# Kernel optimization log

Measured on AMD Instinct MI355X. Metric: run time of the kernel, lower is better.

The kernel has to match this reference:

```python
import jax, jax.numpy as jnp
import numpy as np

TOP_K = 2


def setup_inputs() -> dict:
    key = jax.random.key(0)
    k0, k1, k2, k3, k4, k5 = jax.random.split(key, 6)
    N, D_IN, D_OUT, H, G = 8192, 1024, 1024, 4096, 3
    E = 2 ** G
    x = jax.random.normal(k0, (N, D_IN), jnp.float32)
    # gate: Linear(in_dim, gate_dim, bias=False) followed by act (ReLU)
    Wg = jax.random.normal(k1, (D_IN, G), jnp.float32) * (1.0 / np.sqrt(D_IN))
    # experts: per-expert 2-layer MLP: Linear(in,hid) + ReLU + Linear(hid,out)
    W1 = jax.random.normal(k2, (E, D_IN, H), jnp.float32) * (1.0 / np.sqrt(D_IN))
    b1 = jax.random.normal(k3, (E, H), jnp.float32) * 0.01
    W2 = jax.random.normal(k4, (E, H, D_OUT), jnp.float32) * (1.0 / np.sqrt(H))
    b2 = jax.random.normal(k5, (E, D_OUT), jnp.float32) * 0.01
    return {"x": x, "Wg": Wg, "W1": W1, "b1": b1, "W2": W2, "b2": b2}


def _hypercube_mask(E, G, dtype):
    # binary(arange(2^G), G) * 2 - 1 : corners of the hypercube in {-1,+1}^G
    codes = jnp.arange(E)
    bits = (codes[:, None] >> jnp.arange(G)[None, :]) & 1  # [E, G]
    return (bits * 2 - 1).astype(dtype)


def reference(x, Wg, W1, b1, W2, b2):
    G = Wg.shape[1]
    E = W1.shape[0]
    N = x.shape[0]
    mask = _hypercube_mask(E, G, x.dtype)                 # [E, G]
    logits = jax.nn.relu(x @ Wg)                          # [N, G]
    scores = logits @ mask.T                              # [N, E] = sum_d logits*mask
    probs = jax.nn.softmax(scores, axis=1)                # softmax over experts
    topv, topi = jax.lax.top_k(probs, TOP_K)              # [N, k]
    topv = topv / topv.sum(axis=-1, keepdims=True)        # renormalize selected probs
    # dense combine weights: zero for non-selected experts (same math as gather/scatter dispatch)
    combine = jnp.zeros((N, E), x.dtype).at[jnp.arange(N)[:, None], topi].set(topv)
    out = jnp.zeros((N, W2.shape[2]), x.dtype)
    for e in range(E):  # small fixed expert count
        h = jax.nn.relu(x @ W1[e] + b1[e])                # [N, H]
        out = out + combine[:, e:e + 1] * (h @ W2[e] + b2[e])
    return out
```

## Files before the change

kernel.cpp:

```cpp
#include <hip/hip_runtime.h>

#define NTOK 8192
#define DIN  1024
#define DOUT 1024
#define HDIM 4096
#define NEXP 8
#define NPAIR (NTOK * 2)

typedef __attribute__((ext_vector_type(8))) short bf16x8;
typedef __attribute__((ext_vector_type(4))) float f32x4;

__device__ __forceinline__ unsigned short f2bf(float f) {
  union { float f; unsigned u; } v; v.f = f;
  unsigned u = v.u;
  unsigned r = (u + 0x7fffu + ((u >> 16) & 1u)) >> 16;
  return (unsigned short)r;
}

__device__ __forceinline__ void gload16(const void* g, void* l) {
  __builtin_amdgcn_global_load_lds(
      (const __attribute__((address_space(1))) unsigned int*)g,
      (__attribute__((address_space(3))) unsigned int*)l, 16, 0, 0);
}

__global__ void gate_kernel(const float* __restrict__ x, const float* __restrict__ Wg,
                            int* __restrict__ cnt, int* __restrict__ ptok,
                            float* __restrict__ pw) {
  const int lane = threadIdx.x & 63;
  const int t = blockIdx.x * 4 + (threadIdx.x >> 6);
  const float* xr = x + (size_t)t * DIN + lane * 16;
  const float* wr = Wg + (size_t)lane * 16 * 3;
  double d0 = 0, d1 = 0, d2 = 0;
#pragma unroll
  for (int j = 0; j < 16; j++) {
    double xv = xr[j];
    d0 += xv * wr[j * 3 + 0];
    d1 += xv * wr[j * 3 + 1];
    d2 += xv * wr[j * 3 + 2];
  }
#pragma unroll
  for (int o = 32; o > 0; o >>= 1) {
    d0 += __shfl_down(d0, o);
    d1 += __shfl_down(d1, o);
    d2 += __shfl_down(d2, o);
  }
  if (lane == 0) {
    double l0 = d0 > 0 ? d0 : 0, l1 = d1 > 0 ? d1 : 0, l2 = d2 > 0 ? d2 : 0;
    double s[NEXP];
#pragma unroll
    for (int e = 0; e < NEXP; e++)
      s[e] = ((e & 1) ? l0 : -l0) + ((e & 2) ? l1 : -l1) + ((e & 4) ? l2 : -l2);
    int e0 = 0;
    for (int e = 1; e < NEXP; e++) if (s[e] > s[e0]) e0 = e;
    int e1 = -1;
    for (int e = 0; e < NEXP; e++) { if (e == e0) continue; if (e1 < 0 || s[e] > s[e1]) e1 = e; }
    double w0 = 1.0 / (1.0 + exp(s[e1] - s[e0]));
    double w1 = 1.0 - w0;
    int p0 = atomicAdd(cnt + e0, 1);
    ptok[e0 * NTOK + p0] = t; pw[e0 * NTOK + p0] = (float)w0;
    int p1 = atomicAdd(cnt + e1, 1);
    ptok[e1 * NTOK + p1] = t; pw[e1 * NTOK + p1] = (float)w1;
  }
}

__global__ void scan_kernel(const int* __restrict__ cnt, int* __restrict__ off) {
  if (threadIdx.x == 0) {
    int a = 0;
    for (int e = 0; e < NEXP; e++) { off[e] = a; a += cnt[e]; }
  }
}

__global__ void cvt_bf16_kernel(const float* __restrict__ src,
                                unsigned short* __restrict__ dst, int n) {
  int i = (blockIdx.x * 256 + threadIdx.x) * 8;
  if (i >= n) return;
  float4 a = *(const float4*)(src + i);
  float4 b = *(const float4*)(src + i + 4);
  __align__(16) unsigned short t[8] = {f2bf(a.x), f2bf(a.y), f2bf(a.z), f2bf(a.w),
                                       f2bf(b.x), f2bf(b.y), f2bf(b.z), f2bf(b.w)};
  *(uint4*)(dst + i) = *(const uint4*)t;
}

__global__ void transpose_cvt(const float* __restrict__ src,
                              unsigned short* __restrict__ dst, int K, int N) {
  __shared__ float tile[64][65];
  const size_t base = (size_t)blockIdx.z * K * N;
  const float* s = src + base;
  unsigned short* d = dst + base;
  int n0 = blockIdx.x * 64, k0 = blockIdx.y * 64;
  for (int idx = threadIdx.x; idx < 64 * 16; idx += 256) {
    int r = idx >> 4, c4 = (idx & 15) * 4;
    float4 v = *(const float4*)(s + (size_t)(k0 + r) * N + n0 + c4);
    tile[r][c4 + 0] = v.x; tile[r][c4 + 1] = v.y;
    tile[r][c4 + 2] = v.z; tile[r][c4 + 3] = v.w;
  }
  __syncthreads();
  for (int idx = threadIdx.x; idx < 64 * 8; idx += 256) {
    int nl = idx >> 3, c8 = (idx & 7) * 8;
    __align__(16) unsigned short tmp[8];
#pragma unroll
    for (int j = 0; j < 8; j++) tmp[j] = f2bf(tile[c8 + j][nl]);
    *(uint4*)(d + (size_t)(n0 + nl) * K + k0 + c8) = *(const uint4*)tmp;
  }
}

__global__ __launch_bounds__(256, 2) void gemm1_kernel(
    const unsigned short* __restrict__ xbf,
    const unsigned short* __restrict__ w1t,
    const float* __restrict__ b1,
    const int* __restrict__ cnt, const int* __restrict__ off,
    const int* __restrict__ ptok,
    unsigned short* __restrict__ h)
{
  const int e = blockIdx.z;
  const int ce = cnt[e];
  const int m0 = blockIdx.y * 128;
  if (m0 >= ce) return;
  const int n0 = blockIdx.x * 128;
  const int oe = off[e];
  __shared__ __align__(16) unsigned short lA[128 * 32];
  __shared__ __align__(16) unsigned short lB[128 * 32];
  const int tid = threadIdx.x;
  const int lane = tid & 63;
  const int wv = tid >> 6;
  const int wr = wv >> 1, wc = wv & 1;

  const int c0 = tid, c1 = tid + 256;
  const int ra0 = c0 >> 2, ra1 = c1 >> 2;
  const int ka0 = (c0 & 3) * 8, ka1 = (c1 & 3) * 8;
  const int ta0 = ptok[e * NTOK + min(m0 + ra0, ce - 1)];
  const int ta1 = ptok[e * NTOK + min(m0 + ra1, ce - 1)];
  const unsigned short* ga0 = xbf + (size_t)ta0 * DIN + ka0;
  const unsigned short* ga1 = xbf + (size_t)ta1 * DIN + ka1;
  const unsigned short* wb = w1t + (size_t)e * HDIM * DIN;
  const unsigned short* gb0 = wb + (size_t)(n0 + ra0) * DIN + ka0;
  const unsigned short* gb1 = wb + (size_t)(n0 + ra1) * DIN + ka1;
  unsigned short* lA0 = lA + c0 * 8;
  unsigned short* lA1 = lA + c1 * 8;
  unsigned short* lB0 = lB + c0 * 8;
  unsigned short* lB1 = lB + c1 * 8;

  f32x4 acc[4][4] = {};
  const int fr = lane & 15;
  const int fk = (lane >> 4) * 8;

  for (int k0 = 0; k0 < DIN; k0 += 32) {
    __syncthreads();
    gload16(ga0 + k0, lA0);
    gload16(ga1 + k0, lA1);
    gload16(gb0 + k0, lB0);
    gload16(gb1 + k0, lB1);
    asm volatile("s_waitcnt vmcnt(0)" ::: "memory");
    __syncthreads();
    bf16x8 a[4], b[4];
#pragma unroll
    for (int i = 0; i < 4; i++)
      a[i] = *(const bf16x8*)(lA + ((wr * 64 + i * 16 + fr) * 32 + fk));
#pragma unroll
    for (int i = 0; i < 4; i++)
      b[i] = *(const bf16x8*)(lB + ((wc * 64 + i * 16 + fr) * 32 + fk));
#pragma unroll
    for (int mi = 0; mi < 4; mi++)
#pragma unroll
      for (int ni = 0; ni < 4; ni++)
        acc[mi][ni] = __builtin_amdgcn_mfma_f32_16x16x32_bf16(a[mi], b[ni], acc[mi][ni], 0, 0, 0);
  }

  const int cr = (lane >> 4) * 4;
  const int cc = lane & 15;
#pragma unroll
  for (int mi = 0; mi < 4; mi++) {
    int rbase = wr * 64 + mi * 16 + cr;
#pragma unroll
    for (int r = 0; r < 4; r++) {
      int grow = m0 + rbase + r;
      if (grow >= ce) continue;
      size_t hoff = (size_t)(oe + grow) * HDIM;
#pragma unroll
      for (int ni = 0; ni < 4; ni++) {
        int col = n0 + wc * 64 + ni * 16 + cc;
        float v = acc[mi][ni][r] + b1[e * HDIM + col];
        h[hoff + col] = f2bf(v > 0.f ? v : 0.f);
      }
    }
  }
}

__global__ __launch_bounds__(256, 2) void gemm2_kernel(
    const unsigned short* __restrict__ h,
    const unsigned short* __restrict__ w2t,
    const float* __restrict__ b2,
    const int* __restrict__ cnt, const int* __restrict__ off,
    const int* __restrict__ ptok, const float* __restrict__ pw,
    float* __restrict__ out)
{
  const int e = blockIdx.z;
  const int ce = cnt[e];
  const int m0 = blockIdx.y * 128;
  if (m0 >= ce) return;
  const int n0 = blockIdx.x * 128;
  const int oe = off[e];
  __shared__ __align__(16) unsigned short lA[128 * 32];
  __shared__ __align__(16) unsigned short lB[128 * 32];
  const int tid = threadIdx.x;
  const int lane = tid & 63;
  const int wv = tid >> 6;
  const int wr = wv >> 1, wc = wv & 1;

  const int c0 = tid, c1 = tid + 256;
  const int ra0 = c0 >> 2, ra1 = c1 >> 2;
  const int ka0 = (c0 & 3) * 8, ka1 = (c1 & 3) * 8;
  const int rc0 = min(m0 + ra0, ce - 1), rc1 = min(m0 + ra1, ce - 1);
  const unsigned short* ga0 = h + (size_t)(oe + rc0) * HDIM + ka0;
  const unsigned short* ga1 = h + (size_t)(oe + rc1) * HDIM + ka1;
  const unsigned short* wb = w2t + (size_t)e * DOUT * HDIM;
  const unsigned short* gb0 = wb + (size_t)(n0 + ra0) * HDIM + ka0;
  const unsigned short* gb1 = wb + (size_t)(n0 + ra1) * HDIM + ka1;
  unsigned short* lA0 = lA + c0 * 8;
  unsigned short* lA1 = lA + c1 * 8;
  unsigned short* lB0 = lB + c0 * 8;
  unsigned short* lB1 = lB + c1 * 8;

  f32x4 acc[4][4] = {};
  const int fr = lane & 15;
  const int fk = (lane >> 4) * 8;

  for (int k0 = 0; k0 < HDIM; k0 += 32) {
    __syncthreads();
    gload16(ga0 + k0, lA0);
    gload16(ga1 + k0, lA1);
    gload16(gb0 + k0, lB0);
    gload16(gb1 + k0, lB1);
    asm volatile("s_waitcnt vmcnt(0)" ::: "memory");
    __syncthreads();
    bf16x8 a[4], b[4];
#pragma unroll
    for (int i = 0; i < 4; i++)
      a[i] = *(const bf16x8*)(lA + ((wr * 64 + i * 16 + fr) * 32 + fk));
#pragma unroll
    for (int i = 0; i < 4; i++)
      b[i] = *(const bf16x8*)(lB + ((wc * 64 + i * 16 + fr) * 32 + fk));
#pragma unroll
    for (int mi = 0; mi < 4; mi++)
#pragma unroll
      for (int ni = 0; ni < 4; ni++)
        acc[mi][ni] = __builtin_amdgcn_mfma_f32_16x16x32_bf16(a[mi], b[ni], acc[mi][ni], 0, 0, 0);
  }

  const int cr = (lane >> 4) * 4;
  const int cc = lane & 15;
#pragma unroll
  for (int mi = 0; mi < 4; mi++) {
    int rbase = wr * 64 + mi * 16 + cr;
#pragma unroll
    for (int r = 0; r < 4; r++) {
      int grow = m0 + rbase + r;
      if (grow >= ce) continue;
      int idx = e * NTOK + grow;
      int token = ptok[idx];
      float w = pw[idx];
#pragma unroll
      for (int ni = 0; ni < 4; ni++) {
        int col = n0 + wc * 64 + ni * 16 + cc;
        float v = (acc[mi][ni][r] + b2[e * DOUT + col]) * w;
        atomicAdd(out + (size_t)token * DOUT + col, v);
      }
    }
  }
}

extern "C" void kernel_launch(void* const* d_in, const int* in_sizes, int n_in,
                              void* d_out, int out_size, void* d_ws, size_t ws_size,
                              hipStream_t stream) {
  const float* x  = (const float*)d_in[0];
  const float* Wg = (const float*)d_in[1];
  const float* W1 = (const float*)d_in[2];
  const float* b1 = (const float*)d_in[3];
  const float* W2 = (const float*)d_in[4];
  const float* b2 = (const float*)d_in[5];
  float* out = (float*)d_out;

  char* ws = (char*)d_ws;
  size_t o = 0;
  auto nxt = [&](size_t b) { char* p = ws + o; o = (o + b + 255) & ~(size_t)255; return p; };
  int* cnt = (int*)nxt(64);
  int* off = (int*)nxt(64);
  int* ptok = (int*)nxt((size_t)NEXP * NTOK * 4);
  float* pw = (float*)nxt((size_t)NEXP * NTOK * 4);
  unsigned short* xbf = (unsigned short*)nxt((size_t)NTOK * DIN * 2);
  unsigned short* w1t = (unsigned short*)nxt((size_t)NEXP * HDIM * DIN * 2);
  unsigned short* w2t = (unsigned short*)nxt((size_t)NEXP * DOUT * HDIM * 2);
  unsigned short* hbuf = (unsigned short*)nxt((size_t)NPAIR * HDIM * 2);

  hipMemsetAsync(cnt, 0, 64, stream);
  hipMemsetAsync(out, 0, (size_t)NTOK * DOUT * 4, stream);

  gate_kernel<<<NTOK / 4, 256, 0, stream>>>(x, Wg, cnt, ptok, pw);
  scan_kernel<<<1, 64, 0, stream>>>(cnt, off);
  cvt_bf16_kernel<<<(NTOK * DIN / 8) / 256, 256, 0, stream>>>(x, xbf, NTOK * DIN);
  transpose_cvt<<<dim3(HDIM / 64, DIN / 64, NEXP), 256, 0, stream>>>(W1, w1t, DIN, HDIM);
  transpose_cvt<<<dim3(DOUT / 64, HDIM / 64, NEXP), 256, 0, stream>>>(W2, w2t, HDIM, DOUT);

  gemm1_kernel<<<dim3(HDIM / 128, NTOK / 128, NEXP), 256, 0, stream>>>(
      xbf, w1t, b1, cnt, off, ptok, hbuf);
  gemm2_kernel<<<dim3(DOUT / 128, NTOK / 128, NEXP), 256, 0, stream>>>(
      hbuf, w2t, b2, cnt, off, ptok, pw, out);
}
```

Baseline: 802.7 us.

## Double-buffer LDS tiles, remap blocks across XCDs, and raise occupancy in expert GEMMs

Both expert GEMM kernels now double-buffer the LDS tiles, so the global-to-LDS load of the next K slice is issued before the MFMA work on the current slice. This is meant to hide memory latency that the single-buffer loop exposed. Block IDs are remapped so that consecutive blocks, which the hardware spreads round-robin across the 8 XCDs, share M tiles within an XCD and get better L2 reuse. Launch bounds rise from 2 to 4 waves per SIMD, which tightens the register budget and could cause spills with the 64-float accumulators.

Result: slower. 834.4 us (+3.9%).

```diff
diff --git a/kernel.cpp b/kernel.cpp
--- a/kernel.cpp
+++ b/kernel.cpp
@@ -104,7 +104,7 @@
   }
 }
 
-__global__ __launch_bounds__(256, 2) void gemm1_kernel(
+__global__ __launch_bounds__(256, 4) void gemm1_kernel(
     const unsigned short* __restrict__ xbf,
     const unsigned short* __restrict__ w1t,
     const float* __restrict__ b1,
@@ -114,12 +114,19 @@
 {
   const int e = blockIdx.z;
   const int ce = cnt[e];
-  const int m0 = blockIdx.y * 128;
+  if (ce == 0) return;
+  const int NT = HDIM / 128;
+  const int bid = blockIdx.x + NT * blockIdx.y;
+  const int xcd = bid & 7;
+  const int j = bid >> 3;
+  const int mt = xcd + 8 * (j / NT);
+  const int nt = j % NT;
+  const int m0 = mt * 128;
   if (m0 >= ce) return;
-  const int n0 = blockIdx.x * 128;
+  const int n0 = nt * 128;
   const int oe = off[e];
-  __shared__ __align__(16) unsigned short lA[128 * 32];
-  __shared__ __align__(16) unsigned short lB[128 * 32];
+  __shared__ __align__(16) unsigned short lA[2][128 * 32];
+  __shared__ __align__(16) unsigned short lB[2][128 * 32];
   const int tid = threadIdx.x;
   const int lane = tid & 63;
   const int wv = tid >> 6;
@@ -135,36 +142,44 @@
   const unsigned short* wb = w1t + (size_t)e * HDIM * DIN;
   const unsigned short* gb0 = wb + (size_t)(n0 + ra0) * DIN + ka0;
   const unsigned short* gb1 = wb + (size_t)(n0 + ra1) * DIN + ka1;
-  unsigned short* lA0 = lA + c0 * 8;
-  unsigned short* lA1 = lA + c1 * 8;
-  unsigned short* lB0 = lB + c0 * 8;
-  unsigned short* lB1 = lB + c1 * 8;
 
   f32x4 acc[4][4] = {};
   const int fr = lane & 15;
   const int fk = (lane >> 4) * 8;
 
-  for (int k0 = 0; k0 < DIN; k0 += 32) {
-    __syncthreads();
-    gload16(ga0 + k0, lA0);
-    gload16(ga1 + k0, lA1);
-    gload16(gb0 + k0, lB0);
-    gload16(gb1 + k0, lB1);
+#define STAGE1(buf, kk)                                   \
+  do {                                                    \
+    gload16(ga0 + (kk), &lA[buf][c0 * 8]);                \
+    gload16(ga1 + (kk), &lA[buf][c1 * 8]);                \
+    gload16(gb0 + (kk), &lB[buf][c0 * 8]);                \
+    gload16(gb1 + (kk), &lB[buf][c1 * 8]);                \
+  } while (0)
+
+#define COMPUTE1(buf)                                                        \
+  do {                                                                       \
+    bf16x8 a[4], b[4];                                                       \
+    _Pragma("unroll") for (int i = 0; i < 4; i++)                            \
+      a[i] = *(const bf16x8*)(&lA[buf][(wr * 64 + i * 16 + fr) * 32 + fk]);  \
+    _Pragma("unroll") for (int i = 0; i < 4; i++)                            \
+      b[i] = *(const bf16x8*)(&lB[buf][(wc * 64 + i * 16 + fr) * 32 + fk]);  \
+    _Pragma("unroll") for (int mi = 0; mi < 4; mi++)                         \
+      _Pragma("unroll") for (int ni = 0; ni < 4; ni++)                       \
+        acc[mi][ni] = __builtin_amdgcn_mfma_f32_16x16x32_bf16(               \
+            a[mi], b[ni], acc[mi][ni], 0, 0, 0);                             \
+  } while (0)
+
+  STAGE1(0, 0);
+  asm volatile("s_waitcnt vmcnt(0)" ::: "memory");
+  __syncthreads();
+  int cur = 0;
+  for (int k0 = 32; k0 < DIN; k0 += 32) {
+    STAGE1(cur ^ 1, k0);
+    COMPUTE1(cur);
     asm volatile("s_waitcnt vmcnt(0)" ::: "memory");
     __syncthreads();
-    bf16x8 a[4], b[4];
-#pragma unroll
-    for (int i = 0; i < 4; i++)
-      a[i] = *(const bf16x8*)(lA + ((wr * 64 + i * 16 + fr) * 32 + fk));
-#pragma unroll
-    for (int i = 0; i < 4; i++)
-      b[i] = *(const bf16x8*)(lB + ((wc * 64 + i * 16 + fr) * 32 + fk));
-#pragma unroll
-    for (int mi = 0; mi < 4; mi++)
-#pragma unroll
-      for (int ni = 0; ni < 4; ni++)
-        acc[mi][ni] = __builtin_amdgcn_mfma_f32_16x16x32_bf16(a[mi], b[ni], acc[mi][ni], 0, 0, 0);
-  }
+    cur ^= 1;
+  }
+  COMPUTE1(cur);
 
   const int cr = (lane >> 4) * 4;
   const int cc = lane & 15;
@@ -186,7 +201,7 @@
   }
 }
 
-__global__ __launch_bounds__(256, 2) void gemm2_kernel(
+__global__ __launch_bounds__(256, 4) void gemm2_kernel(
     const unsigned short* __restrict__ h,
     const unsigned short* __restrict__ w2t,
     const float* __restrict__ b2,
@@ -196,12 +211,19 @@
 {
   const int e = blockIdx.z;
   const int ce = cnt[e];
-  const int m0 = blockIdx.y * 128;
+  if (ce == 0) return;
+  const int NT = DOUT / 128;
+  const int bid = blockIdx.x + NT * blockIdx.y;
+  const int xcd = bid & 7;
+  const int j = bid >> 3;
+  const int mt = xcd + 8 * (j / NT);
+  const int nt = j % NT;
+  const int m0 = mt * 128;
   if (m0 >= ce) return;
-  const int n0 = blockIdx.x * 128;
+  const int n0 = nt * 128;
   const int oe = off[e];
-  __shared__ __align__(16) unsigned short lA[128 * 32];
-  __shared__ __align__(16) unsigned short lB[128 * 32];
+  __shared__ __align__(16) unsigned short lA[2][128 * 32];
+  __shared__ __align__(16) unsigned short lB[2][128 * 32];
   const int tid = threadIdx.x;
   const int lane = tid & 63;
   const int wv = tid >> 6;
@@ -216,30 +238,51 @@
   const unsigned short* wb = w2t + (size_t)e * DOUT * HDIM;
   const unsigned short* gb0 = wb + (size_t)(n0 + ra0) * HDIM + ka0;
   const unsigned short* gb1 = wb + (size_t)(n0 + ra1) * HDIM + ka1;
-  unsigned short* lA0 = lA + c0 * 8;
-  unsigned short* lA1 = lA + c1 * 8;
-  unsigned short* lB0 = lB + c0 * 8;
-  unsigned short* lB1 = lB + c1 * 8;
 
   f32x4 acc[4][4] = {};
   const int fr = lane & 15;
   const int fk = (lane >> 4) * 8;
 
-  for (int k0 = 0; k0 < HDIM; k0 += 32) {
-    __syncthreads();
-    gload16(ga0 + k0, lA0);
-    gload16(ga1 + k0, lA1);
-    gload16(gb0 + k0, lB0);
-    gload16(gb1 + k0, lB1);
+#define STAGE2(buf, kk)                                   \
+  do {                                                    \
+    gload16(ga0 + (kk), &lA[buf][c0 * 8]);                \
+    gload16(ga1 + (kk), &lA[buf][c1 * 8]);                \
+    gload16(gb0 + (kk), &lB[buf][c0 * 8]);                \
+    gload16(gb1 + (kk), &lB[buf][c1 * 8]);                \
+  } while (0)
+
+  STAGE2(0, 0);
+  asm volatile("s_waitcnt vmcnt(0)" ::: "memory");
+  __syncthreads();
+  int cur = 0;
+  for (int k0 = 32; k0 < HDIM; k0 += 32) {
+    STAGE2(cur ^ 1, k0);
+    {
+      bf16x8 a[4], b[4];
+#pragma unroll
+      for (int i = 0; i < 4; i++)
+        a[i] = *(const bf16x8*)(&lA[cur][(wr * 64 + i * 16 + fr) * 32 + fk]);
+#pragma unroll
+      for (int i = 0; i < 4; i++)
+        b[i] = *(const bf16x8*)(&lB[cur][(wc * 64 + i * 16 + fr) * 32 + fk]);
+#pragma unroll
+      for (int mi = 0; mi < 4; mi++)
+#pragma unroll
+        for (int ni = 0; ni < 4; ni++)
+          acc[mi][ni] = __builtin_amdgcn_mfma_f32_16x16x32_bf16(a[mi], b[ni], acc[mi][ni], 0, 0, 0);
+    }
     asm volatile("s_waitcnt vmcnt(0)" ::: "memory");
     __syncthreads();
+    cur ^= 1;
+  }
+  {
     bf16x8 a[4], b[4];
 #pragma unroll
     for (int i = 0; i < 4; i++)
-      a[i] = *(const bf16x8*)(lA + ((wr * 64 + i * 16 + fr) * 32 + fk));
+      a[i] = *(const bf16x8*)(&lA[cur][(wr * 64 + i * 16 + fr) * 32 + fk]);
 #pragma unroll
     for (int i = 0; i < 4; i++)
-      b[i] = *(const bf16x8*)(lB + ((wc * 64 + i * 16 + fr) * 32 + fk));
+      b[i] = *(const bf16x8*)(&lB[cur][(wc * 64 + i * 16 + fr) * 32 + fk]);
 #pragma unroll
     for (int mi = 0; mi < 4; mi++)
 #pragma unroll
```
